# Kernel optimization log

Measured on AMD Instinct MI355X. Metric: run time of the kernel, lower is better.

Reference implementation:

```python
import jax, jax.numpy as jnp
import numpy as np

SMOOTH = 1.0
MAX_DIST = 10


def _neighbor_conv(x):
    # 3x3 ones kernel with zero center, padding=1 (NCHW, C=1)
    k = jnp.ones((1, 1, 3, 3), x.dtype).at[0, 0, 1, 1].set(0.0)
    return jax.lax.conv_general_dilated(
        x, k, window_strides=(1, 1), padding=[(1, 1), (1, 1)],
        dimension_numbers=('NCHW', 'OIHW', 'NCHW'))


def _analyze_skeleton(skel):
    n = _neighbor_conv(skel)
    on = skel > 0.5
    endpoints = ((n == 1) & on).astype(skel.dtype)
    midpoints = ((n == 2) & on).astype(skel.dtype)
    junctions = ((n > 2) & on).astype(skel.dtype)
    return endpoints, midpoints, junctions


def _iou(p, g):
    inter = jnp.sum(p * g, axis=(2, 3))
    union = jnp.sum(p, axis=(2, 3)) + jnp.sum(g, axis=(2, 3)) - inter
    return (inter + SMOOTH) / (union + SMOOTH)


def _structural_similarity(pred_skel, gt_skel):
    pe, pm, pj = _analyze_skeleton(pred_skel)
    ge, gm, gj = _analyze_skeleton(gt_skel)
    e_iou, m_iou, j_iou = _iou(pe, ge), _iou(pm, gm), _iou(pj, gj)
    ge_c = jnp.sum(ge, axis=(2, 3))
    gj_c = jnp.sum(gj, axis=(2, 3))
    gm_c = jnp.sum(gm, axis=(2, 3))
    total = ge_c + gj_c + gm_c + SMOOTH
    loss = 1.0 - ((ge_c / total) * e_iou + (gj_c / total) * j_iou + (gm_c / total) * m_iou)
    return loss.mean()


def _maxpool3(x):
    return jax.lax.reduce_window(
        x, -jnp.inf, jax.lax.max,
        window_dimensions=(1, 1, 3, 3), window_strides=(1, 1, 1, 1),
        padding=[(0, 0), (0, 0), (1, 1), (1, 1)])


def _distance_approximation(target, reference):
    # Fixed MAX_DIST iterations; identical math to the torch early-exit loop
    # because new_points requires ~found_mask (no distance is overwritten).
    tgt_on = target > 0.5

    def step(carry, d):
        dilated, found, dist = carry
        dilated = _maxpool3(dilated)
        new = (dilated > 0.5) & tgt_on & (~found)
        dist = dist + d.astype(dist.dtype) * new.astype(dist.dtype)
        return (dilated, found | new, dist), None

    init = (reference, jnp.zeros(target.shape, bool), jnp.zeros_like(target))
    (_, found, dist), _ = jax.lax.scan(step, init, jnp.arange(1, MAX_DIST + 1, dtype=jnp.int32))
    unfound = tgt_on & (~found)
    dist = dist + jnp.asarray(MAX_DIST, dist.dtype) * unfound.astype(dist.dtype)
    total_points = jnp.sum(tgt_on.astype(dist.dtype), axis=(2, 3))
    return jnp.sum(dist, axis=(2, 3)) / (total_points + SMOOTH)


def _medial_axis_distance(pred_skel, gt_skel):
    p2g = _distance_approximation(pred_skel, gt_skel)
    g2p = _distance_approximation(gt_skel, pred_skel)
    return (((p2g + g2p) / 2.0) / MAX_DIST).mean()


def setup_inputs() -> dict:
    key = jax.random.key(0)
    k1, k2 = jax.random.split(key)
    B, C, H, W = 32, 1, 512, 512
    pred_skel = jax.random.uniform(k1, (B, C, H, W), dtype=jnp.float32)
    gt_skel = (jax.random.uniform(k2, (B, C, H, W), dtype=jnp.float32) < 0.1).astype(jnp.float32)
    return {"pred_skel": pred_skel, "gt_skel": gt_skel}


def reference(pred_skel, gt_skel):
    inter = jnp.sum(pred_skel * gt_skel, axis=(2, 3))
    psum = jnp.sum(pred_skel, axis=(2, 3))
    gsum = jnp.sum(gt_skel, axis=(2, 3))
    dice = (2.0 * inter + SMOOTH) / (psum + gsum + SMOOTH)
    dice_loss = 1.0 - dice.mean()
    structural_loss = _structural_similarity(pred_skel, gt_skel)
    medial_loss = _medial_axis_distance(pred_skel, gt_skel)
    avg_mag = (dice_loss + structural_loss + medial_loss) / 3.0
    bal_dice = dice_loss / (dice_loss + SMOOTH) * avg_mag
    bal_struct = structural_loss / (structural_loss + SMOOTH) * avg_mag
    bal_medial = medial_loss / (medial_loss + SMOOTH) * avg_mag
    return bal_dice + bal_struct + bal_medial
```

## Files before the change

### kernel.cpp

```cpp
#include <hip/hip_runtime.h>
#include <stdint.h>

#define BATCH 32
#define H 512
#define W 512
#define NACC 16
#define TH 32
#define HALO 9
#define RH (TH + 2*HALO)
#define RHP 64
#define NT 512
#define NW (NT/64)


__global__ __launch_bounds__(NT, 4) void fused_kernel(
    const float* __restrict__ pred, const float* __restrict__ gt,
    float* __restrict__ acc)
{
    __shared__ uint64_t Mp[2][RHP][8];
    __shared__ uint64_t Mg[2][RHP][8];
    __shared__ float    EC[2][TH];
    __shared__ float    red[NW][16];

    int tile = blockIdx.x, b = blockIdx.y;
    const float* pimg = pred + (size_t)b * H * W;
    const float* gimg = gt   + (size_t)b * H * W;
    int y0 = tile * TH;
    int tid = threadIdx.x, lane = tid & 63, wid = tid >> 6;

    float v0 = 0.f, v1 = 0.f;

    for (int s = wid; s < RH * 8; s += 2 * NW) {
        int rA = s >> 3, segA = s & 7;
        int rB = (s + NW) >> 3, segB = (s + NW) & 7;
        int ryA = y0 - HALO + rA, ryB = y0 - HALO + rB;
        float vpA = 0.f, vgA = 0.f, vpB = 0.f, vgB = 0.f;
        if ((unsigned)ryA < (unsigned)H) {
            int idx = ryA * W + segA * 64 + lane;
            vpA = pimg[idx]; vgA = gimg[idx];
        }
        if ((unsigned)ryB < (unsigned)H) {
            int idx = ryB * W + segB * 64 + lane;
            vpB = pimg[idx]; vgB = gimg[idx];
        }
        unsigned long long mpA = __ballot(vpA > 0.5f);
        unsigned long long mgA = __ballot(vgA > 0.5f);
        unsigned long long mpB = __ballot(vpB > 0.5f);
        unsigned long long mgB = __ballot(vgB > 0.5f);
        if (lane == 0) {
            Mp[0][rA][segA] = mpA; Mg[0][rA][segA] = mgA;
            Mp[0][rB][segB] = mpB; Mg[0][rB][segB] = mgB;
        }
        if (rA >= HALO && rA < HALO + TH) { v1 += vpA; v0 += (vgA > 0.5f) ? vpA : 0.f; }
        if (rB >= HALO && rB < HALO + TH) { v1 += vpB; v0 += (vgB > 0.5f) ? vpB : 0.f; }
    }
    if (tid < (RHP - RH) * 8) {
        int r = RH + (tid >> 3), w = tid & 7;
        Mp[0][r][w] = 0ULL; Mg[0][r][w] = 0ULL;
    }
    if (tid < 64) {
        int c = tid >> 5, r = tid & 31;
        int y = y0 + r, col = 255 + c;
        float sum = (y > 0     ? pimg[(size_t)(y - 1) * W + col] : 0.f)
                  +              pimg[(size_t)y * W + col]
                  + (y < H - 1 ? pimg[(size_t)(y + 1) * W + col] : 0.f);
        EC[c][r] = sum;
    }
    __syncthreads();

    uint64_t Tp = 0ULL, Tg = 0ULL;
    if (tid < 256) {
        int r = HALO + (tid >> 3), w = tid & 7;
        Tp = Mp[0][r][w]; Tg = Mg[0][r][w];
    }
    int dcnt_p = __popcll(Tp), dcnt_g = __popcll(Tg);
    int dsum_p = dcnt_p, dsum_g = dcnt_g;

    float c3=0,c4=0,c5=0,c6=0,c7=0,c8=0,c9=0,c10=0,c11=0;
    {
        int qi = tid & 127, h = tid >> 7;
        int x4 = qi * 4;
        int wdx = qi >> 4;
        int ss = (qi & 15) * 4;
        int ys = y0 + h * 8;

        auto win6 = [&](int rb) -> uint32_t {
            const uint64_t* row = Mg[0][rb];
            uint64_t bm = row[wdx];
            if (ss == 0) {
                uint64_t lo = wdx ? row[wdx - 1] : 0ULL;
                return (uint32_t)(((bm << 1) | (lo >> 63)) & 0x3FULL);
            }
            uint32_t v = (uint32_t)((bm >> (ss - 1)) & 0x3FULL);
            if (ss == 60) {
                uint64_t hi = (wdx < 7) ? row[wdx + 1] : 0ULL;
                v |= ((uint32_t)hi & 1u) << 5;
            }
            return v;
        };

        int rb0 = h * 8 + 8;
        uint32_t wU = win6(rb0), wM = win6(rb0 + 1);

        float4 pm4, pc4;
        {
            bool hm = ys > 0;
            pm4 = hm ? *(const float4*)(pimg + (size_t)(ys - 1) * W + x4)
                     : make_float4(0, 0, 0, 0);
            pc4 = *(const float4*)(pimg + (size_t)ys * W + x4);
        }
        for (int r = 0; r < 8; ++r) {
            int y = ys + r;
            float4 pp4 = (y < H - 1) ? *(const float4*)(pimg + (size_t)(y + 1) * W + x4)
                                     : make_float4(0, 0, 0, 0);
            uint32_t wD = win6(rb0 + 2 + r);
            int ry = h * 8 + r;

            float ps[6];
            ps[1] = pm4.x + pc4.x + pp4.x; ps[2] = pm4.y + pc4.y + pp4.y;
            ps[3] = pm4.z + pc4.z + pp4.z; ps[4] = pm4.w + pc4.w + pp4.w;
            float psl = __shfl_up(ps[4], 1, 64);
            float psr = __shfl_down(ps[1], 1, 64);
            if (lane == 0)  psl = (qi == 0)   ? 0.f : EC[0][ry];
            if (lane == 63) psr = (qi == 127) ? 0.f : EC[1][ry];
            ps[0] = psl; ps[5] = psr;

            float pcv[4] = {pc4.x, pc4.y, pc4.z, pc4.w};
            #pragma unroll
            for (int j = 0; j < 4; ++j) {
                float np = ps[j] + ps[j + 1] + ps[j + 2] - pcv[j];
                bool pon = pcv[j] > 0.5f;
                bool pe  = pon && (np == 1.f);
                bool pmb = pon && (np == 2.f);
                bool pjb = pon && (np > 2.f);
                uint32_t n9 = ((wU >> j) & 7u) | (((wM >> j) & 7u) << 3) | (((wD >> j) & 7u) << 6);
                uint32_t cen = (wM >> (j + 1)) & 1u;
                int ng = __popc(n9) - (int)cen;
                bool gon = cen != 0u;
                bool ge  = gon && (ng == 1);
                bool gmb = gon && (ng == 2);
                bool gjb = gon && (ng > 2);
                c3 += pe;  c4 += pmb;  c5 += pjb;
                c6 += ge;  c7 += gmb;  c8 += gjb;
                c9  += (pe && ge);
                c10 += (pmb && gmb);
                c11 += (pjb && gjb);
            }
            pm4 = pc4; pc4 = pp4; wU = wM; wM = wD;
        }
    }

    int cur = 0;
    int rr = tid >> 3, ww = tid & 7;
    int rc = HALO + (tid >> 3), wc = tid & 7;
    for (int a = 1; a <= 9; ++a) {
        uint64_t up, md, dn;
        up = rr ? Mp[cur][rr - 1][ww] : 0ULL;
        md = Mp[cur][rr][ww];
        dn = (rr < RHP - 1) ? Mp[cur][rr + 1][ww] : 0ULL;
        uint64_t Xp = up | md | dn;
        up = rr ? Mg[cur][rr - 1][ww] : 0ULL;
        md = Mg[cur][rr][ww];
        dn = (rr < RHP - 1) ? Mg[cur][rr + 1][ww] : 0ULL;
        uint64_t Xg = up | md | dn;

        uint32_t lmp = __shfl_up  ((uint32_t)(Xp >> 63), 1, 64);
        uint32_t rlp = __shfl_down((uint32_t)(Xp & 1ULL), 1, 64);
        uint32_t lmg = __shfl_up  ((uint32_t)(Xg >> 63), 1, 64);
        uint32_t rlg = __shfl_down((uint32_t)(Xg & 1ULL), 1, 64);

        uint64_t Yp = Xp | (Xp << 1) | (Xp >> 1);
        uint64_t Yg = Xg | (Xg << 1) | (Xg >> 1);
        if (ww > 0) { Yp |= (uint64_t)(lmp & 1u); Yg |= (uint64_t)(lmg & 1u); }
        if (ww < 7) { Yp |= ((uint64_t)(rlp & 1u)) << 63; Yg |= ((uint64_t)(rlg & 1u)) << 63; }
        Mp[cur ^ 1][rr][ww] = Yp;
        Mg[cur ^ 1][rr][ww] = Yg;
        __syncthreads();
        cur ^= 1;
        if (tid < 256) {
            dsum_p += __popcll(Tp & ~Mg[cur][rc][wc]);
            dsum_g += __popcll(Tg & ~Mp[cur][rc][wc]);
        }
    }

    float vals[16];
    vals[0] = v0; vals[1] = v1; vals[2] = (float)dcnt_g;
    vals[3] = c3; vals[4] = c4; vals[5] = c5;
    vals[6] = c6; vals[7] = c7; vals[8] = c8;
    vals[9] = c9; vals[10] = c10; vals[11] = c11;
    vals[12] = (float)dsum_p; vals[13] = (float)dcnt_p;
    vals[14] = (float)dsum_g; vals[15] = (float)dcnt_g;
    #pragma unroll
    for (int j = 0; j < 16; ++j)
        #pragma unroll
        for (int off = 32; off; off >>= 1)
            vals[j] += __shfl_down(vals[j], off, 64);
    if (lane == 0) {
        #pragma unroll
        for (int j = 0; j < 16; ++j) red[wid][j] = vals[j];
    }
    __syncthreads();
    if (tid < 16) {
        float s = 0.f;
        #pragma unroll
        for (int wv = 0; wv < NW; ++wv) s += red[wv][tid];
        atomicAdd(&acc[b * NACC + tid], s);
    }
}

__global__ __launch_bounds__(64) void final_kernel(
    const float* __restrict__ acc, float* __restrict__ out)
{
    int b = threadIdx.x;
    float dice = 0.f, sloss = 0.f, med = 0.f;
    if (b < BATCH) {
        const float* a = acc + b * NACC;
        float inter = a[0], ps = a[1], gs = a[2];
        dice = (2.f * inter + 1.f) / (ps + gs + 1.f);

        float pe = a[3], pm = a[4], pj = a[5];
        float ge = a[6], gm = a[7], gj = a[8];
        float ie = a[9], im = a[10], ij = a[11];
        float e_iou = (ie + 1.f) / (pe + ge - ie + 1.f);
        float m_iou = (im + 1.f) / (pm + gm - im + 1.f);
        float j_iou = (ij + 1.f) / (pj + gj - ij + 1.f);
        float total = ge + gj + gm + 1.f;
        sloss = 1.f - ((ge / total) * e_iou + (gj / total) * j_iou + (gm / total) * m_iou);

        float p2g = a[12] / (a[13] + 1.f);
        float g2p = a[14] / (a[15] + 1.f);
        med = ((p2g + g2p) * 0.5f) / 10.f;
    }
    #pragma unroll
    for (int off = 32; off; off >>= 1) {
        dice  += __shfl_down(dice,  off, 64);
        sloss += __shfl_down(sloss, off, 64);
        med   += __shfl_down(med,   off, 64);
    }
    if (threadIdx.x == 0) {
        float dice_loss  = 1.f - dice / (float)BATCH;
        float structural = sloss / (float)BATCH;
        float medial     = med / (float)BATCH;
        float avg = (dice_loss + structural + medial) / 3.f;
        float r = dice_loss  / (dice_loss  + 1.f) * avg
                + structural / (structural + 1.f) * avg
                + medial     / (medial     + 1.f) * avg;
        out[0] = r;
    }
}

extern "C" void kernel_launch(void* const* d_in, const int* in_sizes, int n_in,
                              void* d_out, int out_size, void* d_ws, size_t ws_size,
                              hipStream_t stream)
{
    const float* pred = (const float*)d_in[0];
    const float* gt   = (const float*)d_in[1];
    float* acc = (float*)d_ws;
    float* out = (float*)d_out;

    hipMemsetAsync(acc, 0, BATCH * NACC * sizeof(float), stream);
    fused_kernel<<<dim3(H / TH, BATCH), NT, 0, stream>>>(pred, gt, acc);
    final_kernel<<<1, 64, 0, stream>>>(acc, out);
}
```

Before: 133.5 us.

## Halve row tile height, swizzle tile order, and fuse final reduction via last-block

Row tiles shrink from 32 to 16 rows, doubling the block count to 1024 and raising the occupancy hint to 8 blocks per CU. Tile indices are swizzled across a flat grid. The separate final kernel is removed: a global counter identifies the last block, which reads the accumulators with atomics and writes the output. The cost is a higher halo-to-tile ratio (34 loaded rows for 16 useful vs 50 for 32), more redundant loads and dilation work, and idle threads in the dilation loop. The gains are more parallelism and one fewer kernel launch.

```diff
diff --git a/kernel.cpp b/kernel.cpp
--- a/kernel.cpp
+++ b/kernel.cpp
@@ -5,24 +5,34 @@
 #define H 512
 #define W 512
 #define NACC 16
-#define TH 32
+#define TH 16
 #define HALO 9
 #define RH (TH + 2*HALO)
-#define RHP 64
 #define NT 512
 #define NW (NT/64)
-
-
-__global__ __launch_bounds__(NT, 4) void fused_kernel(
+#define NTILE (H/TH)
+#define NBLK (NTILE*BATCH)
+
+
+__device__ __forceinline__ float ld_acc(float* p) {
+    return atomicAdd(p, 0.0f);
+}
+
+__global__ __launch_bounds__(NT, 8) void fused_kernel(
     const float* __restrict__ pred, const float* __restrict__ gt,
-    float* __restrict__ acc)
+    float* __restrict__ acc, float* __restrict__ out)
 {
-    __shared__ uint64_t Mp[2][RHP][8];
-    __shared__ uint64_t Mg[2][RHP][8];
+    __shared__ uint64_t Mp[2][RH][8];
+    __shared__ uint64_t Mg[2][RH][8];
     __shared__ float    EC[2][TH];
     __shared__ float    red[NW][16];
-
-    int tile = blockIdx.x, b = blockIdx.y;
+    __shared__ unsigned int isLast;
+
+    int fid = blockIdx.x;
+    int b   = fid >> 5;
+    int t5  = fid & 31;
+    int tile = ((t5 & 7) << 2) | (t5 >> 3);
+
     const float* pimg = pred + (size_t)b * H * W;
     const float* gimg = gt   + (size_t)b * H * W;
     int y0 = tile * TH;
@@ -54,12 +64,8 @@
         if (rA >= HALO && rA < HALO + TH) { v1 += vpA; v0 += (vgA > 0.5f) ? vpA : 0.f; }
         if (rB >= HALO && rB < HALO + TH) { v1 += vpB; v0 += (vgB > 0.5f) ? vpB : 0.f; }
     }
-    if (tid < (RHP - RH) * 8) {
-        int r = RH + (tid >> 3), w = tid & 7;
-        Mp[0][r][w] = 0ULL; Mg[0][r][w] = 0ULL;
-    }
-    if (tid < 64) {
-        int c = tid >> 5, r = tid & 31;
+    if (tid < 2 * TH) {
+        int c = tid >> 4, r = tid & (TH - 1);
         int y = y0 + r, col = 255 + c;
         float sum = (y > 0     ? pimg[(size_t)(y - 1) * W + col] : 0.f)
                   +              pimg[(size_t)y * W + col]
@@ -69,7 +75,7 @@
     __syncthreads();
 
     uint64_t Tp = 0ULL, Tg = 0ULL;
-    if (tid < 256) {
+    if (tid < TH * 8) {
         int r = HALO + (tid >> 3), w = tid & 7;
         Tp = Mp[0][r][w]; Tg = Mg[0][r][w];
     }
@@ -82,7 +88,7 @@
         int x4 = qi * 4;
         int wdx = qi >> 4;
         int ss = (qi & 15) * 4;
-        int ys = y0 + h * 8;
+        int ys = y0 + h * 4;
 
         auto win6 = [&](int rb) -> uint32_t {
             const uint64_t* row = Mg[0][rb];
@@ -99,7 +105,7 @@
             return v;
         };
 
-        int rb0 = h * 8 + 8;
+        int rb0 = h * 4 + HALO - 1;
         uint32_t wU = win6(rb0), wM = win6(rb0 + 1);
 
         float4 pm4, pc4;
@@ -109,12 +115,12 @@
                      : make_float4(0, 0, 0, 0);
             pc4 = *(const float4*)(pimg + (size_t)ys * W + x4);
         }
-        for (int r = 0; r < 8; ++r) {
+        for (int r = 0; r < 4; ++r) {
             int y = ys + r;
             float4 pp4 = (y < H - 1) ? *(const float4*)(pimg + (size_t)(y + 1) * W + x4)
                                      : make_float4(0, 0, 0, 0);
             uint32_t wD = win6(rb0 + 2 + r);
-            int ry = h * 8 + r;
+            int ry = h * 4 + r;
 
             float ps[6];
             ps[1] = pm4.x + pc4.x + pp4.x; ps[2] = pm4.y + pc4.y + pp4.y;
@@ -151,33 +157,36 @@
     }
 
     int cur = 0;
+    bool active = tid < RH * 8;
     int rr = tid >> 3, ww = tid & 7;
     int rc = HALO + (tid >> 3), wc = tid & 7;
     for (int a = 1; a <= 9; ++a) {
-        uint64_t up, md, dn;
-        up = rr ? Mp[cur][rr - 1][ww] : 0ULL;
-        md = Mp[cur][rr][ww];
-        dn = (rr < RHP - 1) ? Mp[cur][rr + 1][ww] : 0ULL;
-        uint64_t Xp = up | md | dn;
-        up = rr ? Mg[cur][rr - 1][ww] : 0ULL;
-        md = Mg[cur][rr][ww];
-        dn = (rr < RHP - 1) ? Mg[cur][rr + 1][ww] : 0ULL;
-        uint64_t Xg = up | md | dn;
-
-        uint32_t lmp = __shfl_up  ((uint32_t)(Xp >> 63), 1, 64);
-        uint32_t rlp = __shfl_down((uint32_t)(Xp & 1ULL), 1, 64);
-        uint32_t lmg = __shfl_up  ((uint32_t)(Xg >> 63), 1, 64);
-        uint32_t rlg = __shfl_down((uint32_t)(Xg & 1ULL), 1, 64);
-
-        uint64_t Yp = Xp | (Xp << 1) | (Xp >> 1);
-        uint64_t Yg = Xg | (Xg << 1) | (Xg >> 1);
-        if (ww > 0) { Yp |= (uint64_t)(lmp & 1u); Yg |= (uint64_t)(lmg & 1u); }
-        if (ww < 7) { Yp |= ((uint64_t)(rlp & 1u)) << 63; Yg |= ((uint64_t)(rlg & 1u)) << 63; }
-        Mp[cur ^ 1][rr][ww] = Yp;
-        Mg[cur ^ 1][rr][ww] = Yg;
+        if (active) {
+            uint64_t up, md, dn;
+            up = rr ? Mp[cur][rr - 1][ww] : 0ULL;
+            md = Mp[cur][rr][ww];
+            dn = (rr < RH - 1) ? Mp[cur][rr + 1][ww] : 0ULL;
+            uint64_t Xp = up | md | dn;
+            up = rr ? Mg[cur][rr - 1][ww] : 0ULL;
+            md = Mg[cur][rr][ww];
+            dn = (rr < RH - 1) ? Mg[cur][rr + 1][ww] : 0ULL;
+            uint64_t Xg = up | md | dn;
+
+            uint32_t lmp = __shfl_up  ((uint32_t)(Xp >> 63), 1, 64);
+            uint32_t rlp = __shfl_down((uint32_t)(Xp & 1ULL), 1, 64);
+            uint32_t lmg = __shfl_up  ((uint32_t)(Xg >> 63), 1, 64);
+            uint32_t rlg = __shfl_down((uint32_t)(Xg & 1ULL), 1, 64);
+
+            uint64_t Yp = Xp | (Xp << 1) | (Xp >> 1);
+            uint64_t Yg = Xg | (Xg << 1) | (Xg >> 1);
+            if (ww > 0) { Yp |= (uint64_t)(lmp & 1u); Yg |= (uint64_t)(lmg & 1u); }
+            if (ww < 7) { Yp |= ((uint64_t)(rlp & 1u)) << 63; Yg |= ((uint64_t)(rlg & 1u)) << 63; }
+            Mp[cur ^ 1][rr][ww] = Yp;
+            Mg[cur ^ 1][rr][ww] = Yg;
+        }
         __syncthreads();
         cur ^= 1;
-        if (tid < 256) {
+        if (tid < TH * 8) {
             dsum_p += __popcll(Tp & ~Mg[cur][rc][wc]);
             dsum_g += __popcll(Tg & ~Mp[cur][rc][wc]);
         }
@@ -206,46 +215,54 @@
         for (int wv = 0; wv < NW; ++wv) s += red[wv][tid];
         atomicAdd(&acc[b * NACC + tid], s);
     }
-}
-
-__global__ __launch_bounds__(64) void final_kernel(
-    const float* __restrict__ acc, float* __restrict__ out)
-{
-    int b = threadIdx.x;
-    float dice = 0.f, sloss = 0.f, med = 0.f;
-    if (b < BATCH) {
-        const float* a = acc + b * NACC;
-        float inter = a[0], ps = a[1], gs = a[2];
-        dice = (2.f * inter + 1.f) / (ps + gs + 1.f);
-
-        float pe = a[3], pm = a[4], pj = a[5];
-        float ge = a[6], gm = a[7], gj = a[8];
-        float ie = a[9], im = a[10], ij = a[11];
-        float e_iou = (ie + 1.f) / (pe + ge - ie + 1.f);
-        float m_iou = (im + 1.f) / (pm + gm - im + 1.f);
-        float j_iou = (ij + 1.f) / (pj + gj - ij + 1.f);
-        float total = ge + gj + gm + 1.f;
-        sloss = 1.f - ((ge / total) * e_iou + (gj / total) * j_iou + (gm / total) * m_iou);
-
-        float p2g = a[12] / (a[13] + 1.f);
-        float g2p = a[14] / (a[15] + 1.f);
-        med = ((p2g + g2p) * 0.5f) / 10.f;
-    }
-    #pragma unroll
-    for (int off = 32; off; off >>= 1) {
-        dice  += __shfl_down(dice,  off, 64);
-        sloss += __shfl_down(sloss, off, 64);
-        med   += __shfl_down(med,   off, 64);
-    }
-    if (threadIdx.x == 0) {
-        float dice_loss  = 1.f - dice / (float)BATCH;
-        float structural = sloss / (float)BATCH;
-        float medial     = med / (float)BATCH;
-        float avg = (dice_loss + structural + medial) / 3.f;
-        float r = dice_loss  / (dice_loss  + 1.f) * avg
-                + structural / (structural + 1.f) * avg
-                + medial     / (medial     + 1.f) * avg;
-        out[0] = r;
+
+    __threadfence();
+    if (tid == 0) {
+        unsigned int t = atomicAdd((unsigned int*)&acc[BATCH * NACC], 1u);
+        isLast = (t == NBLK - 1) ? 1u : 0u;
+    }
+    __syncthreads();
+    if (isLast && tid < 64) {
+        __threadfence();
+        int bb = tid;
+        float dice = 0.f, sloss = 0.f, med = 0.f;
+        if (bb < BATCH) {
+            float* a = acc + bb * NACC;
+            float av[16];
+            #pragma unroll
+            for (int j = 0; j < 16; ++j) av[j] = ld_acc(&a[j]);
+            float inter = av[0], psum = av[1], gsum = av[2];
+            dice = (2.f * inter + 1.f) / (psum + gsum + 1.f);
+
+            float pe = av[3], pm = av[4], pj = av[5];
+            float ge = av[6], gm = av[7], gj = av[8];
+            float ie = av[9], im = av[10], ij = av[11];
+            float e_iou = (ie + 1.f) / (pe + ge - ie + 1.f);
+            float m_iou = (im + 1.f) / (pm + gm - im + 1.f);
+            float j_iou = (ij + 1.f) / (pj + gj - ij + 1.f);
+            float total = ge + gj + gm + 1.f;
+            sloss = 1.f - ((ge / total) * e_iou + (gj / total) * j_iou + (gm / total) * m_iou);
+
+            float p2g = av[12] / (av[13] + 1.f);
+            float g2p = av[14] / (av[15] + 1.f);
+            med = ((p2g + g2p) * 0.5f) / 10.f;
+        }
+        #pragma unroll
+        for (int off = 32; off; off >>= 1) {
+            dice  += __shfl_down(dice,  off, 64);
+            sloss += __shfl_down(sloss, off, 64);
+            med   += __shfl_down(med,   off, 64);
+        }
+        if (tid == 0) {
+            float dice_loss  = 1.f - dice / (float)BATCH;
+            float structural = sloss / (float)BATCH;
+            float medial     = med / (float)BATCH;
+            float avg = (dice_loss + structural + medial) / 3.f;
+            float r = dice_loss  / (dice_loss  + 1.f) * avg
+                    + structural / (structural + 1.f) * avg
+                    + medial     / (medial     + 1.f) * avg;
+            out[0] = r;
+        }
     }
 }
 
@@ -258,7 +275,6 @@
     float* acc = (float*)d_ws;
     float* out = (float*)d_out;
 
-    hipMemsetAsync(acc, 0, BATCH * NACC * sizeof(float), stream);
-    fused_kernel<<<dim3(H / TH, BATCH), NT, 0, stream>>>(pred, gt, acc);
-    final_kernel<<<1, 64, 0, stream>>>(acc, out);
+    hipMemsetAsync(acc, 0, (BATCH * NACC + 1) * sizeof(float), stream);
+    fused_kernel<<<dim3(NBLK), NT, 0, stream>>>(pred, gt, acc, out);
 }
```

Measured after the change: 344.5 us. 2.58x slower.
